# Performance work log

Measured on AMD Instinct MI355X. Metric: run time of the kernel, lower is better.

Reference implementation:

```python
import jax, jax.numpy as jnp
import numpy as np

N_NODES = 50000
N_EDGES = 600000
D_IN = 128
DIMS = [128, 128, 128]
LEAKY_SLOPE = 0.01  # torch nn.LeakyReLU default


def setup_inputs() -> dict:
    key = jax.random.key(0)
    ks = jax.random.split(key, 10)
    feat = jax.random.uniform(ks[0], (N_NODES, D_IN), dtype=jnp.float32) + 1e-3
    edge_index = jax.random.randint(ks[1], (2, N_EDGES), 0, N_NODES, dtype=jnp.int64)
    edge_weight = jax.random.uniform(ks[2], (N_EDGES,), dtype=jnp.float32) + 1e-3
    # 3 GCNConv layers: x @ W ([c_in, c_out]) then scatter-aggregate, then + bias
    scale1 = 1.0 / np.sqrt(D_IN)
    W1 = jax.random.normal(ks[3], (D_IN, DIMS[0]), dtype=jnp.float32) * scale1
    b1 = jnp.zeros((DIMS[0],), dtype=jnp.float32)
    W2 = jax.random.normal(ks[4], (DIMS[0], DIMS[1]), dtype=jnp.float32) * (1.0 / np.sqrt(DIMS[0]))
    b2 = jnp.zeros((DIMS[1],), dtype=jnp.float32)
    W3 = jax.random.normal(ks[5], (DIMS[1], DIMS[2]), dtype=jnp.float32) * (1.0 / np.sqrt(DIMS[1]))
    b3 = jnp.zeros((DIMS[2],), dtype=jnp.float32)
    return {"feat": feat, "edge_index": edge_index, "edge_weight": edge_weight,
            "W1": W1, "b1": b1, "W2": W2, "b2": b2, "W3": W3, "b3": b3}


def reference(feat, edge_index, edge_weight, W1, b1, W2, b2, W3, b3):
    N = feat.shape[0]
    src = edge_index[0]  # edge (i, j): A[i, j]; messages flow src -> dst
    dst = edge_index[1]
    # A_hat = D^{-1} A D^{-1}, D = diag(row sums of A)
    rowsum = jax.ops.segment_sum(edge_weight, src, num_segments=N)
    rinv = jnp.where(rowsum > 0, 1.0 / rowsum, 0.0)
    w_hat = edge_weight * rinv[src] * rinv[dst]
    # PyG gcn_norm (add_self_loops=False): deg over target, symmetric D^{-1/2} scaling
    deg = jax.ops.segment_sum(w_hat, dst, num_segments=N)
    dinv = jnp.where(deg > 0, jax.lax.rsqrt(deg), 0.0)
    norm = dinv[src] * w_hat * dinv[dst]  # cached, shared by all layers

    def gcn_conv(x, W, b):
        x = x @ W                              # [N, c_out]
        msg = norm[:, None] * x[src]           # gather + scale: [E, c_out]
        agg = jax.ops.segment_sum(msg, dst, num_segments=N)  # scatter-add
        return agg + b

    x = feat / jnp.sum(feat, axis=1, keepdims=True)  # row-normalize
    x = jax.nn.leaky_relu(gcn_conv(x, W1, b1), LEAKY_SLOPE)
    x = jax.nn.leaky_relu(gcn_conv(x, W2, b2), LEAKY_SLOPE)
    x = gcn_conv(x, W3, b3)  # final layer: no activation
    return x
```

## Files before the change

kernel.cpp:

```cpp
#include <hip/hip_runtime.h>

#define D 128
#define LEAKY 0.01f
#define SCAN_CHUNK 2048

typedef __attribute__((ext_vector_type(8))) short short8;
typedef __attribute__((ext_vector_type(4))) float f32x4;

__device__ __forceinline__ unsigned short f2bf(float f) {
    unsigned u = __float_as_uint(f);
    u += 0x7fffu + ((u >> 16) & 1u);
    return (unsigned short)(u >> 16);
}


__global__ void k_wprep(const float* __restrict__ W1, const float* __restrict__ W2,
                        const float* __restrict__ W3, unsigned short* __restrict__ wtg) {
    int tid = blockIdx.x * 256 + threadIdx.x;
    if (tid >= 3 * 128 * 16) return;
    int col = tid & 127;
    int s   = (tid >> 7) & 15;
    int w   = tid >> 11;
    const float* Ws = (w == 0) ? W1 : (w == 1) ? W2 : W3;
    unsigned un[4];
    #pragma unroll
    for (int p = 0; p < 4; p++) {
        float a = Ws[(s * 8 + 2 * p) * 128 + col];
        float b = Ws[(s * 8 + 2 * p + 1) * 128 + col];
        un[p] = (unsigned)f2bf(a) | ((unsigned)f2bf(b) << 16);
    }
    uint4 v = {un[0], un[1], un[2], un[3]};
    int byte = w * 32768 + col * 256 + ((s * 16) ^ ((col & 7) << 4));
    *(uint4*)((char*)wtg + byte) = v;
}


__global__ void k_pass1(const int* __restrict__ src, const int* __restrict__ dst,
                        const float* __restrict__ w, float* __restrict__ rowsum,
                        int* __restrict__ cnt, int* __restrict__ rank, int E) {
    int e = blockIdx.x * 256 + threadIdx.x;
    if (e >= E) return;
    atomicAdd(&rowsum[src[e]], w[e]);
    rank[e] = atomicAdd(&cnt[dst[e]], 1);
}


__global__ void k_chunk_sum(const int* __restrict__ cnt, int* __restrict__ partial, int n) {
    __shared__ int sdata[256];
    int b = blockIdx.x;
    int base = b * SCAN_CHUNK;
    int s = 0;
    for (int i = threadIdx.x; i < SCAN_CHUNK; i += 256) {
        int idx = base + i;
        s += (idx < n) ? cnt[idx] : 0;
    }
    sdata[threadIdx.x] = s;
    __syncthreads();
    for (int off = 128; off > 0; off >>= 1) {
        if (threadIdx.x < off) sdata[threadIdx.x] += sdata[threadIdx.x + off];
        __syncthreads();
    }
    if (threadIdx.x == 0) partial[b] = sdata[0];
}

__global__ void k_scan_partial(int* __restrict__ partial, int nchunks) {
    if (blockIdx.x == 0 && threadIdx.x == 0) {
        int run = 0;
        for (int i = 0; i < nchunks; i++) { int v = partial[i]; partial[i] = run; run += v; }
    }
}

__global__ void k_chunk_scan(const int* __restrict__ cnt, const int* __restrict__ partial,
                             int* __restrict__ start, int n, int total) {
    __shared__ int sdata[256];
    int b = blockIdx.x;
    int base = b * SCAN_CHUNK;
    int t = threadIdx.x;
    int loc[8];
    int s = 0;
    int tb = base + t * 8;
    #pragma unroll
    for (int j = 0; j < 8; j++) {
        int idx = tb + j;
        int v = (idx < n) ? cnt[idx] : 0;
        loc[j] = s;
        s += v;
    }
    sdata[t] = s;
    __syncthreads();
    for (int off = 1; off < 256; off <<= 1) {
        int v = (t >= off) ? sdata[t - off] : 0;
        __syncthreads();
        sdata[t] += v;
        __syncthreads();
    }
    int texcl = (t == 0) ? 0 : sdata[t - 1];
    int offb = partial[b];
    #pragma unroll
    for (int j = 0; j < 8; j++) {
        int idx = tb + j;
        if (idx < n) start[idx] = offb + texcl + loc[j];
    }
    if (b == gridDim.x - 1 && t == 255) start[n] = total;
}


__global__ void k_scatter2(const int* __restrict__ src, const int* __restrict__ dst,
                           const float* __restrict__ w, const float* __restrict__ rowsum,
                           const int* __restrict__ start, const int* __restrict__ rank,
                           int2* __restrict__ csr, int E) {
    int e = blockIdx.x * 256 + threadIdx.x;
    if (e >= E) return;
    int s = src[e], d = dst[e];
    float rs = rowsum[s], rd = rowsum[d];
    float wh = w[e] * (rs > 0.f ? 1.f / rs : 0.f) * (rd > 0.f ? 1.f / rd : 0.f);
    int idx = start[d] + rank[e];
    csr[idx] = make_int2(s, __float_as_int(wh));
}


__global__ void k_deg_dinv(const int2* __restrict__ csr, const int* __restrict__ start,
                           float* __restrict__ dinv, int N) {
    int n = blockIdx.x * 256 + threadIdx.x;
    if (n >= N) return;
    int s0 = start[n], s1 = start[n + 1];
    float s = 0.f;
    for (int i = s0; i < s1; i++) s += __int_as_float(csr[i].y);
    dinv[n] = s > 0.f ? rsqrtf(s) : 0.f;
}


#define GR 64

template<int DO_NORM>
__global__ __launch_bounds__(256) void k_gemm_mfma(const float* __restrict__ Xf32,
                                                   const unsigned short* __restrict__ Xb,
                                                   const unsigned short* __restrict__ Wtg,
                                                   unsigned short* __restrict__ Yb, int nrows) {
    __shared__ unsigned short Wt[128 * 128];
    __shared__ unsigned short Xs[GR * 128];
    int t = threadIdx.x;
    int rowbase = blockIdx.x * GR;

    {
        const uint4* Wg = (const uint4*)Wtg;
        uint4* Wl = (uint4*)Wt;
        #pragma unroll
        for (int i = 0; i < 8; i++) Wl[t + i * 256] = Wg[t + i * 256];
    }

    if (DO_NORM) {
        int r = t >> 2, q = t & 3;
        int row = rowbase + r;
        const float4* Xr = (const float4*)(Xf32 + (size_t)row * 128);
        float4 v[8];
        float s = 0.f;
        #pragma unroll
        for (int k = 0; k < 8; k++) {
            float4 x = make_float4(0.f, 0.f, 0.f, 0.f);
            if (row < nrows) x = Xr[q + k * 4];
            v[k] = x;
            s += x.x + x.y + x.z + x.w;
        }
        s += __shfl_down(s, 2, 4);
        s += __shfl_down(s, 1, 4);
        float tot = __shfl(s, 0, 4);
        float inv = tot > 0.f ? 1.f / tot : 0.f;
        int sw = (r & 7) << 4;
        #pragma unroll
        for (int k = 0; k < 8; k++) {
            int gidx = q + k * 4;
            ushort4 h;
            h.x = f2bf(v[k].x * inv); h.y = f2bf(v[k].y * inv);
            h.z = f2bf(v[k].z * inv); h.w = f2bf(v[k].w * inv);
            *(ushort4*)((char*)Xs + r * 256 + ((gidx * 8) ^ sw)) = h;
        }
    } else {
        for (int i = t; i < GR * 16; i += 256) {
            int r = i >> 4, c = i & 15;
            uint4 vv = {0u, 0u, 0u, 0u};
            int row = rowbase + r;
            if (row < nrows) vv = *(const uint4*)(Xb + (size_t)row * 128 + c * 8);
            int byte = r * 256 + ((c * 16) ^ ((r & 7) << 4));
            *(uint4*)((char*)Xs + byte) = vv;
        }
    }
    __syncthreads();

    int w = t >> 6, l = t & 63;
    int r0 = w * 16;
    int lr = l & 15, lg = l >> 4;

    short8 a[4];
    {
        int row = r0 + lr;
        const char* rp = (const char*)Xs + row * 256;
        int sw = (row & 7) << 4;
        #pragma unroll
        for (int s = 0; s < 4; s++)
            a[s] = *(const short8*)(rp + ((s * 64 + lg * 16) ^ sw));
    }

    f32x4 acc[8];
    #pragma unroll
    for (int ct = 0; ct < 8; ct++) {
        f32x4 c = {0.f, 0.f, 0.f, 0.f};
        int col = ct * 16 + lr;
        const char* cp = (const char*)Wt + col * 256;
        int sw = (col & 7) << 4;
        #pragma unroll
        for (int s = 0; s < 4; s++) {
            short8 b = *(const short8*)(cp + ((s * 64 + lg * 16) ^ sw));
            c = __builtin_amdgcn_mfma_f32_16x16x32_bf16(a[s], b, c, 0, 0, 0);
        }
        acc[ct] = c;
    }

    #pragma unroll
    for (int j = 0; j < 4; j++) {
        int row = rowbase + r0 + lg * 4 + j;
        if (row < nrows) {
            #pragma unroll
            for (int ct = 0; ct < 8; ct++)
                Yb[(size_t)row * 128 + ct * 16 + lr] = f2bf(acc[ct][j]);
        }
    }
}


__device__ __forceinline__ void fma8(float* acc, float n, uint4 v) {
    acc[0] += n * __uint_as_float(v.x << 16);
    acc[1] += n * __uint_as_float(v.x & 0xffff0000u);
    acc[2] += n * __uint_as_float(v.y << 16);
    acc[3] += n * __uint_as_float(v.y & 0xffff0000u);
    acc[4] += n * __uint_as_float(v.z << 16);
    acc[5] += n * __uint_as_float(v.z & 0xffff0000u);
    acc[6] += n * __uint_as_float(v.w << 16);
    acc[7] += n * __uint_as_float(v.w & 0xffff0000u);
}

template<int NORM, int FINAL>
__global__ void k_agg(const unsigned short* __restrict__ Yb, int2* __restrict__ csr,
                      const int* __restrict__ start, const float* __restrict__ dinv,
                      const float* __restrict__ bias,
                      unsigned short* __restrict__ OutB, float* __restrict__ OutF, int N) {
    int wid = (blockIdx.x * blockDim.x + threadIdx.x) >> 6;
    int lane = threadIdx.x & 63;
    int g = lane >> 4;
    int l = lane & 15;
    int node = wid * 4 + g;
    bool valid = node < N;
    int s0 = valid ? start[node] : 0;
    int s1 = valid ? start[node + 1] : 0;
    int cnt = s1 - s0;
    float ddst = 0.f;
    if (NORM) ddst = valid ? dinv[node] : 0.f;

    float acc[8] = {};
    const uint4* Y4 = (const uint4*)Yb;

    for (int base = 0; base < cnt; base += 16) {
        int rem = cnt - base; if (rem > 16) rem = 16;
        int eidx = s0 + base + l;
        int2 pr = (l < rem) ? csr[eidx] : make_int2(0, 0);
        int  sj = pr.x;
        float nj = __int_as_float(pr.y);
        if (NORM) {
            nj = nj * dinv[sj] * ddst;
            if (l < rem) csr[eidx] = make_int2(sj, __float_as_int(nj));
        }
        int j = 0;
        for (; j + 8 <= rem; j += 8) {
            int   i0 = __shfl(sj, j + 0, 16), i1 = __shfl(sj, j + 1, 16);
            int   i2 = __shfl(sj, j + 2, 16), i3 = __shfl(sj, j + 3, 16);
            int   i4 = __shfl(sj, j + 4, 16), i5 = __shfl(sj, j + 5, 16);
            int   i6 = __shfl(sj, j + 6, 16), i7 = __shfl(sj, j + 7, 16);
            float n0 = __shfl(nj, j + 0, 16), n1 = __shfl(nj, j + 1, 16);
            float n2 = __shfl(nj, j + 2, 16), n3 = __shfl(nj, j + 3, 16);
            float n4 = __shfl(nj, j + 4, 16), n5 = __shfl(nj, j + 5, 16);
            float n6 = __shfl(nj, j + 6, 16), n7 = __shfl(nj, j + 7, 16);
            uint4 v0 = Y4[(size_t)i0 * 16 + l];
            uint4 v1 = Y4[(size_t)i1 * 16 + l];
            uint4 v2 = Y4[(size_t)i2 * 16 + l];
            uint4 v3 = Y4[(size_t)i3 * 16 + l];
            uint4 v4 = Y4[(size_t)i4 * 16 + l];
            uint4 v5 = Y4[(size_t)i5 * 16 + l];
            uint4 v6 = Y4[(size_t)i6 * 16 + l];
            uint4 v7 = Y4[(size_t)i7 * 16 + l];
            fma8(acc, n0, v0); fma8(acc, n1, v1);
            fma8(acc, n2, v2); fma8(acc, n3, v3);
            fma8(acc, n4, v4); fma8(acc, n5, v5);
            fma8(acc, n6, v6); fma8(acc, n7, v7);
        }
        for (; j + 4 <= rem; j += 4) {
            int   i0 = __shfl(sj, j + 0, 16), i1 = __shfl(sj, j + 1, 16);
            int   i2 = __shfl(sj, j + 2, 16), i3 = __shfl(sj, j + 3, 16);
            float n0 = __shfl(nj, j + 0, 16), n1 = __shfl(nj, j + 1, 16);
            float n2 = __shfl(nj, j + 2, 16), n3 = __shfl(nj, j + 3, 16);
            uint4 v0 = Y4[(size_t)i0 * 16 + l];
            uint4 v1 = Y4[(size_t)i1 * 16 + l];
            uint4 v2 = Y4[(size_t)i2 * 16 + l];
            uint4 v3 = Y4[(size_t)i3 * 16 + l];
            fma8(acc, n0, v0); fma8(acc, n1, v1);
            fma8(acc, n2, v2); fma8(acc, n3, v3);
        }
        for (; j < rem; j++) {
            int   i0 = __shfl(sj, j, 16);
            float n0 = __shfl(nj, j, 16);
            uint4 v0 = Y4[(size_t)i0 * 16 + l];
            fma8(acc, n0, v0);
        }
    }

    if (!valid) return;
    float4 ba = ((const float4*)bias)[l * 2];
    float4 bb = ((const float4*)bias)[l * 2 + 1];
    float o[8];
    o[0] = acc[0] + ba.x; o[1] = acc[1] + ba.y; o[2] = acc[2] + ba.z; o[3] = acc[3] + ba.w;
    o[4] = acc[4] + bb.x; o[5] = acc[5] + bb.y; o[6] = acc[6] + bb.z; o[7] = acc[7] + bb.w;
    if (FINAL) {
        float4 w0 = {o[0], o[1], o[2], o[3]};
        float4 w1 = {o[4], o[5], o[6], o[7]};
        ((float4*)OutF)[(size_t)node * 32 + l * 2] = w0;
        ((float4*)OutF)[(size_t)node * 32 + l * 2 + 1] = w1;
    } else {
        #pragma unroll
        for (int k = 0; k < 8; k++) o[k] = o[k] > 0.f ? o[k] : LEAKY * o[k];
        uint4 ov;
        ov.x = (unsigned)f2bf(o[0]) | ((unsigned)f2bf(o[1]) << 16);
        ov.y = (unsigned)f2bf(o[2]) | ((unsigned)f2bf(o[3]) << 16);
        ov.z = (unsigned)f2bf(o[4]) | ((unsigned)f2bf(o[5]) << 16);
        ov.w = (unsigned)f2bf(o[6]) | ((unsigned)f2bf(o[7]) << 16);
        ((uint4*)OutB)[(size_t)node * 16 + l] = ov;
    }
}


extern "C" void kernel_launch(void* const* d_in, const int* in_sizes, int n_in,
                              void* d_out, int out_size, void* d_ws, size_t ws_size,
                              hipStream_t stream) {
    const float* feat = (const float*)d_in[0];
    const int*   eidx = (const int*)d_in[1];
    const float* ew   = (const float*)d_in[2];
    const float* W1   = (const float*)d_in[3];
    const float* b1   = (const float*)d_in[4];
    const float* W2   = (const float*)d_in[5];
    const float* b2   = (const float*)d_in[6];
    const float* W3   = (const float*)d_in[7];
    const float* b3   = (const float*)d_in[8];

    const int N = in_sizes[0] / D;
    const int E = in_sizes[2];
    const int* src = eidx;
    const int* dst = eidx + E;

    size_t off = 0;
    char* base = (char*)d_ws;
    auto alloc4 = [&](size_t elems) -> void* {
        void* p = base + off * 4;
        off += (elems + 3) & ~(size_t)3;
        return p;
    };
    float* rowsum = (float*)alloc4(N);
    int*   cnt    = (int*)  alloc4(N);
    char*  zero_end = base + off * 4;
    int*   start  = (int*)  alloc4(N + 1);
    float* dinv   = (float*)alloc4(N);
    int*   partial= (int*)  alloc4(64);
    int*   rank   = (int*)  alloc4(E);
    int2*  csr    = (int2*) alloc4((size_t)E * 2);
    unsigned short* wtg = (unsigned short*)alloc4(24576);
    unsigned short* xb  = (unsigned short*)alloc4((size_t)N * 64);
    unsigned short* yb  = (unsigned short*)alloc4((size_t)N * 64);
    float* outp = (float*)d_out;

    hipMemsetAsync(rowsum, 0, (size_t)(zero_end - (char*)rowsum), stream);

    int eblocks = (E + 255) / 256;
    int nchunks = (N + SCAN_CHUNK - 1) / SCAN_CHUNK;
    int nblocks = (N + 255) / 256;
    int ablocks = (((N + 3) / 4) * 64 + 255) / 256;
    int gblocks = (N + GR - 1) / GR;

    k_wprep<<<24, 256, 0, stream>>>(W1, W2, W3, wtg);
    k_pass1<<<eblocks, 256, 0, stream>>>(src, dst, ew, rowsum, cnt, rank, E);

    k_chunk_sum<<<nchunks, 256, 0, stream>>>(cnt, partial, N);
    k_scan_partial<<<1, 64, 0, stream>>>(partial, nchunks);
    k_chunk_scan<<<nchunks, 256, 0, stream>>>(cnt, partial, start, N, E);

    k_scatter2<<<eblocks, 256, 0, stream>>>(src, dst, ew, rowsum, start, rank, csr, E);
    k_deg_dinv<<<nblocks, 256, 0, stream>>>(csr, start, dinv, N);

    k_gemm_mfma<1><<<gblocks, 256, 0, stream>>>(feat, nullptr, wtg, xb, N);
    k_agg<1, 0><<<ablocks, 256, 0, stream>>>(xb, csr, start, dinv, b1, yb, nullptr, N);
    k_gemm_mfma<0><<<gblocks, 256, 0, stream>>>(nullptr, yb, wtg + 16384, yb, N);
    k_agg<0, 0><<<ablocks, 256, 0, stream>>>(yb, csr, start, nullptr, b2, xb, nullptr, N);
    k_gemm_mfma<0><<<gblocks, 256, 0, stream>>>(nullptr, xb, wtg + 32768, xb, N);
    k_agg<0, 1><<<ablocks, 256, 0, stream>>>(xb, csr, start, nullptr, b3, nullptr, outp, N);
}
```

Baseline: 302.0 us.

## Fuse aggregation with next layer's GEMM via shared-memory tile

Aggregation for layers 1 and 2 is merged with the following layer's MFMA GEMM. Each block aggregates 64 nodes, applies bias and LeakyReLU, writes the bf16 rows into a swizzled LDS tile, then multiplies by the next weight matrix. This removes one intermediate global write/read and two kernel launches. In exchange, blocks now hold 48KB of LDS and each 16-lane group walks four nodes in sequence, which reduces parallelism for the latency-bound gather.

```diff
diff --git a/kernel.cpp b/kernel.cpp
--- a/kernel.cpp
+++ b/kernel.cpp
@@ -130,104 +130,6 @@
 }
 
 
-#define GR 64
-
-template<int DO_NORM>
-__global__ __launch_bounds__(256) void k_gemm_mfma(const float* __restrict__ Xf32,
-                                                   const unsigned short* __restrict__ Xb,
-                                                   const unsigned short* __restrict__ Wtg,
-                                                   unsigned short* __restrict__ Yb, int nrows) {
-    __shared__ unsigned short Wt[128 * 128];
-    __shared__ unsigned short Xs[GR * 128];
-    int t = threadIdx.x;
-    int rowbase = blockIdx.x * GR;
-
-    {
-        const uint4* Wg = (const uint4*)Wtg;
-        uint4* Wl = (uint4*)Wt;
-        #pragma unroll
-        for (int i = 0; i < 8; i++) Wl[t + i * 256] = Wg[t + i * 256];
-    }
-
-    if (DO_NORM) {
-        int r = t >> 2, q = t & 3;
-        int row = rowbase + r;
-        const float4* Xr = (const float4*)(Xf32 + (size_t)row * 128);
-        float4 v[8];
-        float s = 0.f;
-        #pragma unroll
-        for (int k = 0; k < 8; k++) {
-            float4 x = make_float4(0.f, 0.f, 0.f, 0.f);
-            if (row < nrows) x = Xr[q + k * 4];
-            v[k] = x;
-            s += x.x + x.y + x.z + x.w;
-        }
-        s += __shfl_down(s, 2, 4);
-        s += __shfl_down(s, 1, 4);
-        float tot = __shfl(s, 0, 4);
-        float inv = tot > 0.f ? 1.f / tot : 0.f;
-        int sw = (r & 7) << 4;
-        #pragma unroll
-        for (int k = 0; k < 8; k++) {
-            int gidx = q + k * 4;
-            ushort4 h;
-            h.x = f2bf(v[k].x * inv); h.y = f2bf(v[k].y * inv);
-            h.z = f2bf(v[k].z * inv); h.w = f2bf(v[k].w * inv);
-            *(ushort4*)((char*)Xs + r * 256 + ((gidx * 8) ^ sw)) = h;
-        }
-    } else {
-        for (int i = t; i < GR * 16; i += 256) {
-            int r = i >> 4, c = i & 15;
-            uint4 vv = {0u, 0u, 0u, 0u};
-            int row = rowbase + r;
-            if (row < nrows) vv = *(const uint4*)(Xb + (size_t)row * 128 + c * 8);
-            int byte = r * 256 + ((c * 16) ^ ((r & 7) << 4));
-            *(uint4*)((char*)Xs + byte) = vv;
-        }
-    }
-    __syncthreads();
-
-    int w = t >> 6, l = t & 63;
-    int r0 = w * 16;
-    int lr = l & 15, lg = l >> 4;
-
-    short8 a[4];
-    {
-        int row = r0 + lr;
-        const char* rp = (const char*)Xs + row * 256;
-        int sw = (row & 7) << 4;
-        #pragma unroll
-        for (int s = 0; s < 4; s++)
-            a[s] = *(const short8*)(rp + ((s * 64 + lg * 16) ^ sw));
-    }
-
-    f32x4 acc[8];
-    #pragma unroll
-    for (int ct = 0; ct < 8; ct++) {
-        f32x4 c = {0.f, 0.f, 0.f, 0.f};
-        int col = ct * 16 + lr;
-        const char* cp = (const char*)Wt + col * 256;
-        int sw = (col & 7) << 4;
-        #pragma unroll
-        for (int s = 0; s < 4; s++) {
-            short8 b = *(const short8*)(cp + ((s * 64 + lg * 16) ^ sw));
-            c = __builtin_amdgcn_mfma_f32_16x16x32_bf16(a[s], b, c, 0, 0, 0);
-        }
-        acc[ct] = c;
-    }
-
-    #pragma unroll
-    for (int j = 0; j < 4; j++) {
-        int row = rowbase + r0 + lg * 4 + j;
-        if (row < nrows) {
-            #pragma unroll
-            for (int ct = 0; ct < 8; ct++)
-                Yb[(size_t)row * 128 + ct * 16 + lr] = f2bf(acc[ct][j]);
-        }
-    }
-}
-
-
 __device__ __forceinline__ void fma8(float* acc, float n, uint4 v) {
     acc[0] += n * __uint_as_float(v.x << 16);
     acc[1] += n * __uint_as_float(v.x & 0xffff0000u);
@@ -239,26 +141,11 @@
     acc[7] += n * __uint_as_float(v.w & 0xffff0000u);
 }
 
-template<int NORM, int FINAL>
-__global__ void k_agg(const unsigned short* __restrict__ Yb, int2* __restrict__ csr,
-                      const int* __restrict__ start, const float* __restrict__ dinv,
-                      const float* __restrict__ bias,
-                      unsigned short* __restrict__ OutB, float* __restrict__ OutF, int N) {
-    int wid = (blockIdx.x * blockDim.x + threadIdx.x) >> 6;
-    int lane = threadIdx.x & 63;
-    int g = lane >> 4;
-    int l = lane & 15;
-    int node = wid * 4 + g;
-    bool valid = node < N;
-    int s0 = valid ? start[node] : 0;
-    int s1 = valid ? start[node + 1] : 0;
-    int cnt = s1 - s0;
-    float ddst = 0.f;
-    if (NORM) ddst = valid ? dinv[node] : 0.f;
-
-    float acc[8] = {};
-    const uint4* Y4 = (const uint4*)Yb;
-
+template<int NORM>
+__device__ __forceinline__ void agg_accum(const uint4* __restrict__ Y4, int2* __restrict__ csr,
+                                          int s0, int cnt, int l,
+                                          const float* __restrict__ dinv, float ddst,
+                                          float* acc) {
     for (int base = 0; base < cnt; base += 16) {
         int rem = cnt - base; if (rem > 16) rem = 16;
         int eidx = s0 + base + l;
@@ -311,19 +198,54 @@
             fma8(acc, n0, v0);
         }
     }
-
-    if (!valid) return;
+}
+
+
+template<int NORM>
+__global__ __launch_bounds__(256) void k_agg_gemm(const unsigned short* __restrict__ Yb_prev,
+                                                  int2* __restrict__ csr,
+                                                  const int* __restrict__ start,
+                                                  const float* __restrict__ dinv,
+                                                  const float* __restrict__ bias,
+                                                  const unsigned short* __restrict__ Wtg,
+                                                  unsigned short* __restrict__ Yb_out, int N) {
+    __shared__ unsigned short Wt[128 * 128];
+    __shared__ unsigned short Xs[64 * 128];
+    int t = threadIdx.x;
+    int rowbase = blockIdx.x * 64;
+
+    {
+        const uint4* Wg = (const uint4*)Wtg;
+        uint4* Wl = (uint4*)Wt;
+        #pragma unroll
+        for (int i = 0; i < 8; i++) Wl[t + i * 256] = Wg[t + i * 256];
+    }
+
+    int lane = t & 63;
+    int wv = t >> 6;
+    int g = lane >> 4;
+    int l = lane & 15;
+    int G = wv * 4 + g;
+    const uint4* Y4 = (const uint4*)Yb_prev;
     float4 ba = ((const float4*)bias)[l * 2];
     float4 bb = ((const float4*)bias)[l * 2 + 1];
-    float o[8];
-    o[0] = acc[0] + ba.x; o[1] = acc[1] + ba.y; o[2] = acc[2] + ba.z; o[3] = acc[3] + ba.w;
-    o[4] = acc[4] + bb.x; o[5] = acc[5] + bb.y; o[6] = acc[6] + bb.z; o[7] = acc[7] + bb.w;
-    if (FINAL) {
-        float4 w0 = {o[0], o[1], o[2], o[3]};
-        float4 w1 = {o[4], o[5], o[6], o[7]};
-        ((float4*)OutF)[(size_t)node * 32 + l * 2] = w0;
-        ((float4*)OutF)[(size_t)node * 32 + l * 2 + 1] = w1;
-    } else {
+
+    for (int i = 0; i < 4; i++) {
+        int r = G * 4 + i;
+        int node = rowbase + r;
+        bool valid = node < N;
+        int s0 = valid ? start[node] : 0;
+        int s1 = valid ? start[node + 1] : 0;
+        int cnt = s1 - s0;
+        float ddst = 0.f;
+        if (NORM) ddst = valid ? dinv[node] : 0.f;
+
+        float acc[8] = {};
+        agg_accum<NORM>(Y4, csr, s0, cnt, l, dinv, ddst, acc);
+
+        float o[8];
+        o[0] = acc[0] + ba.x; o[1] = acc[1] + ba.y; o[2] = acc[2] + ba.z; o[3] = acc[3] + ba.w;
+        o[4] = acc[4] + bb.x; o[5] = acc[5] + bb.y; o[6] = acc[6] + bb.z; o[7] = acc[7] + bb.w;
         #pragma unroll
         for (int k = 0; k < 8; k++) o[k] = o[k] > 0.f ? o[k] : LEAKY * o[k];
         uint4 ov;
@@ -331,8 +253,161 @@
         ov.y = (unsigned)f2bf(o[2]) | ((unsigned)f2bf(o[3]) << 16);
         ov.z = (unsigned)f2bf(o[4]) | ((unsigned)f2bf(o[5]) << 16);
         ov.w = (unsigned)f2bf(o[6]) | ((unsigned)f2bf(o[7]) << 16);
-        ((uint4*)OutB)[(size_t)node * 16 + l] = ov;
-    }
+        int byte = r * 256 + ((l * 16) ^ ((r & 7) << 4));
+        *(uint4*)((char*)Xs + byte) = ov;
+    }
+    __syncthreads();
+
+    int r0 = wv * 16;
+    int lr = lane & 15, lg = lane >> 4;
+
+    short8 a[4];
+    {
+        int row = r0 + lr;
+        const char* rp = (const char*)Xs + row * 256;
+        int sw = (row & 7) << 4;
+        #pragma unroll
+        for (int s = 0; s < 4; s++)
+            a[s] = *(const short8*)(rp + ((s * 64 + lg * 16) ^ sw));
+    }
+
+    f32x4 accv[8];
+    #pragma unroll
+    for (int ct = 0; ct < 8; ct++) {
+        f32x4 c = {0.f, 0.f, 0.f, 0.f};
+        int col = ct * 16 + lr;
+        const char* cp = (const char*)Wt + col * 256;
+        int sw = (col & 7) << 4;
+        #pragma unroll
+        for (int s = 0; s < 4; s++) {
+            short8 b = *(const short8*)(cp + ((s * 64 + lg * 16) ^ sw));
+            c = __builtin_amdgcn_mfma_f32_16x16x32_bf16(a[s], b, c, 0, 0, 0);
+        }
+        accv[ct] = c;
+    }
+
+    #pragma unroll
+    for (int j = 0; j < 4; j++) {
+        int row = rowbase + r0 + lg * 4 + j;
+        if (row < N) {
+            #pragma unroll
+            for (int ct = 0; ct < 8; ct++)
+                Yb_out[(size_t)row * 128 + ct * 16 + lr] = f2bf(accv[ct][j]);
+        }
+    }
+}
+
+
+#define GR 64
+
+__global__ __launch_bounds__(256) void k_gemm1(const float* __restrict__ Xf32,
+                                               const unsigned short* __restrict__ Wtg,
+                                               unsigned short* __restrict__ Yb, int nrows) {
+    __shared__ unsigned short Wt[128 * 128];
+    __shared__ unsigned short Xs[GR * 128];
+    int t = threadIdx.x;
+    int rowbase = blockIdx.x * GR;
+
+    {
+        const uint4* Wg = (const uint4*)Wtg;
+        uint4* Wl = (uint4*)Wt;
+        #pragma unroll
+        for (int i = 0; i < 8; i++) Wl[t + i * 256] = Wg[t + i * 256];
+    }
+
+    {
+        int r = t >> 2, q = t & 3;
+        int row = rowbase + r;
+        const float4* Xr = (const float4*)(Xf32 + (size_t)row * 128);
+        float4 v[8];
+        float s = 0.f;
+        #pragma unroll
+        for (int k = 0; k < 8; k++) {
+            float4 x = make_float4(0.f, 0.f, 0.f, 0.f);
+            if (row < nrows) x = Xr[q + k * 4];
+            v[k] = x;
+            s += x.x + x.y + x.z + x.w;
+        }
+        s += __shfl_down(s, 2, 4);
+        s += __shfl_down(s, 1, 4);
+        float tot = __shfl(s, 0, 4);
+        float inv = tot > 0.f ? 1.f / tot : 0.f;
+        int sw = (r & 7) << 4;
+        #pragma unroll
+        for (int k = 0; k < 8; k++) {
+            int gidx = q + k * 4;
+            ushort4 h;
+            h.x = f2bf(v[k].x * inv); h.y = f2bf(v[k].y * inv);
+            h.z = f2bf(v[k].z * inv); h.w = f2bf(v[k].w * inv);
+            *(ushort4*)((char*)Xs + r * 256 + ((gidx * 8) ^ sw)) = h;
+        }
+    }
+    __syncthreads();
+
+    int w = t >> 6, l = t & 63;
+    int r0 = w * 16;
+    int lr = l & 15, lg = l >> 4;
+
+    short8 a[4];
+    {
+        int row = r0 + lr;
+        const char* rp = (const char*)Xs + row * 256;
+        int sw = (row & 7) << 4;
+        #pragma unroll
+        for (int s = 0; s < 4; s++)
+            a[s] = *(const short8*)(rp + ((s * 64 + lg * 16) ^ sw));
+    }
+
+    f32x4 acc[8];
+    #pragma unroll
+    for (int ct = 0; ct < 8; ct++) {
+        f32x4 c = {0.f, 0.f, 0.f, 0.f};
+        int col = ct * 16 + lr;
+        const char* cp = (const char*)Wt + col * 256;
+        int sw = (col & 7) << 4;
+        #pragma unroll
+        for (int s = 0; s < 4; s++) {
+            short8 b = *(const short8*)(cp + ((s * 64 + lg * 16) ^ sw));
+            c = __builtin_amdgcn_mfma_f32_16x16x32_bf16(a[s], b, c, 0, 0, 0);
+        }
+        acc[ct] = c;
+    }
+
+    #pragma unroll
+    for (int j = 0; j < 4; j++) {
+        int row = rowbase + r0 + lg * 4 + j;
+        if (row < nrows) {
+            #pragma unroll
+            for (int ct = 0; ct < 8; ct++)
+                Yb[(size_t)row * 128 + ct * 16 + lr] = f2bf(acc[ct][j]);
+        }
+    }
+}
+
+
+__global__ void k_agg_final(const unsigned short* __restrict__ Yb, int2* __restrict__ csr,
+                            const int* __restrict__ start, const float* __restrict__ bias,
+                            float* __restrict__ OutF, int N) {
+    int wid = (blockIdx.x * blockDim.x + threadIdx.x) >> 6;
+    int lane = threadIdx.x & 63;
+    int g = lane >> 4;
+    int l = lane & 15;
+    int node = wid * 4 + g;
+    bool valid = node < N;
+    int s0 = valid ? start[node] : 0;
+    int s1 = valid ? start[node + 1] : 0;
+    int cnt = s1 - s0;
+
+    float acc[8] = {};
+    agg_accum<0>((const uint4*)Yb, csr, s0, cnt, l, nullptr, 0.f, acc);
+
+    if (!valid) return;
+    float4 ba = ((const float4*)bias)[l * 2];
+    float4 bb = ((const float4*)bias)[l * 2 + 1];
+    float4 w0 = {acc[0] + ba.x, acc[1] + ba.y, acc[2] + ba.z, acc[3] + ba.w};
+    float4 w1 = {acc[4] + bb.x, acc[5] + bb.y, acc[6] + bb.z, acc[7] + bb.w};
+    ((float4*)OutF)[(size_t)node * 32 + l * 2] = w0;
+    ((float4*)OutF)[(size_t)node * 32 + l * 2 + 1] = w1;
 }
 
 
@@ -380,7 +455,7 @@
     int nchunks = (N + SCAN_CHUNK - 1) / SCAN_CHUNK;
     int nblocks = (N + 255) / 256;
     int ablocks = (((N + 3) / 4) * 64 + 255) / 256;
-    int gblocks = (N + GR - 1) / GR;
+    int gblocks = (N + 63) / 64;
 
     k_wprep<<<24, 256, 0, stream>>>(W1, W2, W3, wtg);
     k_pass1<<<eblocks, 256, 0, stream>>>(src, dst, ew, rowsum, cnt, rank, E);
@@ -392,10 +467,8 @@
     k_scatter2<<<eblocks, 256, 0, stream>>>(src, dst, ew, rowsum, start, rank, csr, E);
     k_deg_dinv<<<nblocks, 256, 0, stream>>>(csr, start, dinv, N);
 
-    k_gemm_mfma<1><<<gblocks, 256, 0, stream>>>(feat, nullptr, wtg, xb, N);
-    k_agg<1, 0><<<ablocks, 256, 0, stream>>>(xb, csr, start, dinv, b1, yb, nullptr, N);
-    k_gemm_mfma<0><<<gblocks, 256, 0, stream>>>(nullptr, yb, wtg + 16384, yb, N);
-    k_agg<0, 0><<<ablocks, 256, 0, stream>>>(yb, csr, start, nullptr, b2, xb, nullptr, N);
-    k_gemm_mfma<0><<<gblocks, 256, 0, stream>>>(nullptr, xb, wtg + 32768, xb, N);
-    k_agg<0, 1><<<ablocks, 256, 0, stream>>>(xb, csr, start, nullptr, b3, nullptr, outp, N);
-}
+    k_gemm1<<<gblocks, 256, 0, stream>>>(feat, wtg, xb, N);
+    k_agg_gemm<1><<<gblocks, 256, 0, stream>>>(xb, csr, start, dinv, b1, wtg + 16384, yb, N);
+    k_agg_gemm<0><<<gblocks, 256, 0, stream>>>(yb, csr, start, nullptr, b2, wtg + 32768, xb, N);
+    k_agg_final<<<ablocks, 256, 0, stream>>>(xb, csr, start, b3, outp, N);
+}
```

Result: slower. 314.3 us (+4.1%).

## Replace stored edge ranks with atomic decrement slots and fully unroll aggregation gathers

Applied to the files above, without the earlier changes.

Pass 1 no longer writes a per-edge rank array. The scatter kernel instead claims a CSR slot by atomically decrementing the per-destination count, which removes a write and a read of an E-sized array at the cost of a second round of atomics. The aggregation inner loop is also replaced by a helper that always issues 16 gathers per chunk, with masked lanes fetching row 0 at weight zero, to raise memory-level parallelism. This makes CSR order within a row nondeterministic and wastes gathers on rows with low degree.

```diff
diff --git a/kernel.cpp b/kernel.cpp
--- a/kernel.cpp
+++ b/kernel.cpp
@@ -37,11 +37,11 @@
 
 __global__ void k_pass1(const int* __restrict__ src, const int* __restrict__ dst,
                         const float* __restrict__ w, float* __restrict__ rowsum,
-                        int* __restrict__ cnt, int* __restrict__ rank, int E) {
+                        int* __restrict__ cnt, int E) {
     int e = blockIdx.x * 256 + threadIdx.x;
     if (e >= E) return;
     atomicAdd(&rowsum[src[e]], w[e]);
-    rank[e] = atomicAdd(&cnt[dst[e]], 1);
+    atomicAdd(&cnt[dst[e]], 1);
 }
 
 
@@ -107,14 +107,15 @@
 
 __global__ void k_scatter2(const int* __restrict__ src, const int* __restrict__ dst,
                            const float* __restrict__ w, const float* __restrict__ rowsum,
-                           const int* __restrict__ start, const int* __restrict__ rank,
+                           const int* __restrict__ start, int* __restrict__ cnt,
                            int2* __restrict__ csr, int E) {
     int e = blockIdx.x * 256 + threadIdx.x;
     if (e >= E) return;
     int s = src[e], d = dst[e];
     float rs = rowsum[s], rd = rowsum[d];
     float wh = w[e] * (rs > 0.f ? 1.f / rs : 0.f) * (rd > 0.f ? 1.f / rd : 0.f);
-    int idx = start[d] + rank[e];
+    int p = atomicSub(&cnt[d], 1) - 1;
+    int idx = start[d] + p;
     csr[idx] = make_int2(s, __float_as_int(wh));
 }
 
@@ -127,104 +128,6 @@
     float s = 0.f;
     for (int i = s0; i < s1; i++) s += __int_as_float(csr[i].y);
     dinv[n] = s > 0.f ? rsqrtf(s) : 0.f;
-}
-
-
-#define GR 64
-
-template<int DO_NORM>
-__global__ __launch_bounds__(256) void k_gemm_mfma(const float* __restrict__ Xf32,
-                                                   const unsigned short* __restrict__ Xb,
-                                                   const unsigned short* __restrict__ Wtg,
-                                                   unsigned short* __restrict__ Yb, int nrows) {
-    __shared__ unsigned short Wt[128 * 128];
-    __shared__ unsigned short Xs[GR * 128];
-    int t = threadIdx.x;
-    int rowbase = blockIdx.x * GR;
-
-    {
-        const uint4* Wg = (const uint4*)Wtg;
-        uint4* Wl = (uint4*)Wt;
-        #pragma unroll
-        for (int i = 0; i < 8; i++) Wl[t + i * 256] = Wg[t + i * 256];
-    }
-
-    if (DO_NORM) {
-        int r = t >> 2, q = t & 3;
-        int row = rowbase + r;
-        const float4* Xr = (const float4*)(Xf32 + (size_t)row * 128);
-        float4 v[8];
-        float s = 0.f;
-        #pragma unroll
-        for (int k = 0; k < 8; k++) {
-            float4 x = make_float4(0.f, 0.f, 0.f, 0.f);
-            if (row < nrows) x = Xr[q + k * 4];
-            v[k] = x;
-            s += x.x + x.y + x.z + x.w;
-        }
-        s += __shfl_down(s, 2, 4);
-        s += __shfl_down(s, 1, 4);
-        float tot = __shfl(s, 0, 4);
-        float inv = tot > 0.f ? 1.f / tot : 0.f;
-        int sw = (r & 7) << 4;
-        #pragma unroll
-        for (int k = 0; k < 8; k++) {
-            int gidx = q + k * 4;
-            ushort4 h;
-            h.x = f2bf(v[k].x * inv); h.y = f2bf(v[k].y * inv);
-            h.z = f2bf(v[k].z * inv); h.w = f2bf(v[k].w * inv);
-            *(ushort4*)((char*)Xs + r * 256 + ((gidx * 8) ^ sw)) = h;
-        }
-    } else {
-        for (int i = t; i < GR * 16; i += 256) {
-            int r = i >> 4, c = i & 15;
-            uint4 vv = {0u, 0u, 0u, 0u};
-            int row = rowbase + r;
-            if (row < nrows) vv = *(const uint4*)(Xb + (size_t)row * 128 + c * 8);
-            int byte = r * 256 + ((c * 16) ^ ((r & 7) << 4));
-            *(uint4*)((char*)Xs + byte) = vv;
-        }
-    }
-    __syncthreads();
-
-    int w = t >> 6, l = t & 63;
-    int r0 = w * 16;
-    int lr = l & 15, lg = l >> 4;
-
-    short8 a[4];
-    {
-        int row = r0 + lr;
-        const char* rp = (const char*)Xs + row * 256;
-        int sw = (row & 7) << 4;
-        #pragma unroll
-        for (int s = 0; s < 4; s++)
-            a[s] = *(const short8*)(rp + ((s * 64 + lg * 16) ^ sw));
-    }
-
-    f32x4 acc[8];
-    #pragma unroll
-    for (int ct = 0; ct < 8; ct++) {
-        f32x4 c = {0.f, 0.f, 0.f, 0.f};
-        int col = ct * 16 + lr;
-        const char* cp = (const char*)Wt + col * 256;
-        int sw = (col & 7) << 4;
-        #pragma unroll
-        for (int s = 0; s < 4; s++) {
-            short8 b = *(const short8*)(cp + ((s * 64 + lg * 16) ^ sw));
-            c = __builtin_amdgcn_mfma_f32_16x16x32_bf16(a[s], b, c, 0, 0, 0);
-        }
-        acc[ct] = c;
-    }
-
-    #pragma unroll
-    for (int j = 0; j < 4; j++) {
-        int row = rowbase + r0 + lg * 4 + j;
-        if (row < nrows) {
-            #pragma unroll
-            for (int ct = 0; ct < 8; ct++)
-                Yb[(size_t)row * 128 + ct * 16 + lr] = f2bf(acc[ct][j]);
-        }
-    }
 }
 
 
@@ -238,6 +141,36 @@
     acc[6] += n * __uint_as_float(v.w << 16);
     acc[7] += n * __uint_as_float(v.w & 0xffff0000u);
 }
+
+template<int NORM>
+__device__ __forceinline__ void agg_accum(const uint4* __restrict__ Y4, int2* __restrict__ csr,
+                                          int s0, int cnt, int l,
+                                          const float* __restrict__ dinv, float ddst,
+                                          float* acc) {
+    for (int base = 0; base < cnt; base += 16) {
+        int rem = cnt - base; if (rem > 16) rem = 16;
+        int eidx = s0 + base + l;
+        int2 pr = (l < rem) ? csr[eidx] : make_int2(0, 0);
+        int  sj = pr.x;
+        float nj = __int_as_float(pr.y);
+        if (NORM) {
+            nj = nj * dinv[sj] * ddst;
+            if (l < rem) csr[eidx] = make_int2(sj, __float_as_int(nj));
+        }
+        int idx[16]; float nn[16];
+        #pragma unroll
+        for (int j = 0; j < 16; j++) {
+            idx[j] = __shfl(sj, j, 16);
+            nn[j]  = __shfl(nj, j, 16);
+        }
+        uint4 v[16];
+        #pragma unroll
+        for (int j = 0; j < 16; j++) v[j] = Y4[(size_t)idx[j] * 16 + l];
+        #pragma unroll
+        for (int j = 0; j < 16; j++) fma8(acc, nn[j], v[j]);
+    }
+}
+
 
 template<int NORM, int FINAL>
 __global__ void k_agg(const unsigned short* __restrict__ Yb, int2* __restrict__ csr,
@@ -257,60 +190,7 @@
     if (NORM) ddst = valid ? dinv[node] : 0.f;
 
     float acc[8] = {};
-    const uint4* Y4 = (const uint4*)Yb;
-
-    for (int base = 0; base < cnt; base += 16) {
-        int rem = cnt - base; if (rem > 16) rem = 16;
-        int eidx = s0 + base + l;
-        int2 pr = (l < rem) ? csr[eidx] : make_int2(0, 0);
-        int  sj = pr.x;
-        float nj = __int_as_float(pr.y);
-        if (NORM) {
-            nj = nj * dinv[sj] * ddst;
-            if (l < rem) csr[eidx] = make_int2(sj, __float_as_int(nj));
-        }
-        int j = 0;
-        for (; j + 8 <= rem; j += 8) {
-            int   i0 = __shfl(sj, j + 0, 16), i1 = __shfl(sj, j + 1, 16);
-            int   i2 = __shfl(sj, j + 2, 16), i3 = __shfl(sj, j + 3, 16);
-            int   i4 = __shfl(sj, j + 4, 16), i5 = __shfl(sj, j + 5, 16);
-            int   i6 = __shfl(sj, j + 6, 16), i7 = __shfl(sj, j + 7, 16);
-            float n0 = __shfl(nj, j + 0, 16), n1 = __shfl(nj, j + 1, 16);
-            float n2 = __shfl(nj, j + 2, 16), n3 = __shfl(nj, j + 3, 16);
-            float n4 = __shfl(nj, j + 4, 16), n5 = __shfl(nj, j + 5, 16);
-            float n6 = __shfl(nj, j + 6, 16), n7 = __shfl(nj, j + 7, 16);
-            uint4 v0 = Y4[(size_t)i0 * 16 + l];
-            uint4 v1 = Y4[(size_t)i1 * 16 + l];
-            uint4 v2 = Y4[(size_t)i2 * 16 + l];
-            uint4 v3 = Y4[(size_t)i3 * 16 + l];
-            uint4 v4 = Y4[(size_t)i4 * 16 + l];
-            uint4 v5 = Y4[(size_t)i5 * 16 + l];
-            uint4 v6 = Y4[(size_t)i6 * 16 + l];
-            uint4 v7 = Y4[(size_t)i7 * 16 + l];
-            fma8(acc, n0, v0); fma8(acc, n1, v1);
-            fma8(acc, n2, v2); fma8(acc, n3, v3);
-            fma8(acc, n4, v4); fma8(acc, n5, v5);
-            fma8(acc, n6, v6); fma8(acc, n7, v7);
-        }
-        for (; j + 4 <= rem; j += 4) {
-            int   i0 = __shfl(sj, j + 0, 16), i1 = __shfl(sj, j + 1, 16);
-            int   i2 = __shfl(sj, j + 2, 16), i3 = __shfl(sj, j + 3, 16);
-            float n0 = __shfl(nj, j + 0, 16), n1 = __shfl(nj, j + 1, 16);
-            float n2 = __shfl(nj, j + 2, 16), n3 = __shfl(nj, j + 3, 16);
-            uint4 v0 = Y4[(size_t)i0 * 16 + l];
-            uint4 v1 = Y4[(size_t)i1 * 16 + l];
-            uint4 v2 = Y4[(size_t)i2 * 16 + l];
-            uint4 v3 = Y4[(size_t)i3 * 16 + l];
-            fma8(acc, n0, v0); fma8(acc, n1, v1);
-            fma8(acc, n2, v2); fma8(acc, n3, v3);
-        }
-        for (; j < rem; j++) {
-            int   i0 = __shfl(sj, j, 16);
-            float n0 = __shfl(nj, j, 16);
-            uint4 v0 = Y4[(size_t)i0 * 16 + l];
-            fma8(acc, n0, v0);
-        }
-    }
+    agg_accum<NORM>((const uint4*)Yb, csr, s0, cnt, l, dinv, ddst, acc);
 
     if (!valid) return;
     float4 ba = ((const float4*)bias)[l * 2];
@@ -332,6 +212,104 @@
         ov.z = (unsigned)f2bf(o[4]) | ((unsigned)f2bf(o[5]) << 16);
         ov.w = (unsigned)f2bf(o[6]) | ((unsigned)f2bf(o[7]) << 16);
         ((uint4*)OutB)[(size_t)node * 16 + l] = ov;
+    }
+}
+
+
+#define GR 64
+
+template<int DO_NORM>
+__global__ __launch_bounds__(256) void k_gemm_mfma(const float* __restrict__ Xf32,
+                                                   const unsigned short* __restrict__ Xb,
+                                                   const unsigned short* __restrict__ Wtg,
+                                                   unsigned short* __restrict__ Yb, int nrows) {
+    __shared__ unsigned short Wt[128 * 128];
+    __shared__ unsigned short Xs[GR * 128];
+    int t = threadIdx.x;
+    int rowbase = blockIdx.x * GR;
+
+    {
+        const uint4* Wg = (const uint4*)Wtg;
+        uint4* Wl = (uint4*)Wt;
+        #pragma unroll
+        for (int i = 0; i < 8; i++) Wl[t + i * 256] = Wg[t + i * 256];
+    }
+
+    if (DO_NORM) {
+        int r = t >> 2, q = t & 3;
+        int row = rowbase + r;
+        const float4* Xr = (const float4*)(Xf32 + (size_t)row * 128);
+        float4 v[8];
+        float s = 0.f;
+        #pragma unroll
+        for (int k = 0; k < 8; k++) {
+            float4 x = make_float4(0.f, 0.f, 0.f, 0.f);
+            if (row < nrows) x = Xr[q + k * 4];
+            v[k] = x;
+            s += x.x + x.y + x.z + x.w;
+        }
+        s += __shfl_down(s, 2, 4);
+        s += __shfl_down(s, 1, 4);
+        float tot = __shfl(s, 0, 4);
+        float inv = tot > 0.f ? 1.f / tot : 0.f;
+        int sw = (r & 7) << 4;
+        #pragma unroll
+        for (int k = 0; k < 8; k++) {
+            int gidx = q + k * 4;
+            ushort4 h;
+            h.x = f2bf(v[k].x * inv); h.y = f2bf(v[k].y * inv);
+            h.z = f2bf(v[k].z * inv); h.w = f2bf(v[k].w * inv);
+            *(ushort4*)((char*)Xs + r * 256 + ((gidx * 8) ^ sw)) = h;
+        }
+    } else {
+        for (int i = t; i < GR * 16; i += 256) {
+            int r = i >> 4, c = i & 15;
+            uint4 vv = {0u, 0u, 0u, 0u};
+            int row = rowbase + r;
+            if (row < nrows) vv = *(const uint4*)(Xb + (size_t)row * 128 + c * 8);
+            int byte = r * 256 + ((c * 16) ^ ((r & 7) << 4));
+            *(uint4*)((char*)Xs + byte) = vv;
+        }
+    }
+    __syncthreads();
+
+    int w = t >> 6, l = t & 63;
+    int r0 = w * 16;
+    int lr = l & 15, lg = l >> 4;
+
+    short8 a[4];
+    {
+        int row = r0 + lr;
+        const char* rp = (const char*)Xs + row * 256;
+        int sw = (row & 7) << 4;
+        #pragma unroll
+        for (int s = 0; s < 4; s++)
+            a[s] = *(const short8*)(rp + ((s * 64 + lg * 16) ^ sw));
+    }
+
+    f32x4 acc[8];
+    #pragma unroll
+    for (int ct = 0; ct < 8; ct++) {
+        f32x4 c = {0.f, 0.f, 0.f, 0.f};
+        int col = ct * 16 + lr;
+        const char* cp = (const char*)Wt + col * 256;
+        int sw = (col & 7) << 4;
+        #pragma unroll
+        for (int s = 0; s < 4; s++) {
+            short8 b = *(const short8*)(cp + ((s * 64 + lg * 16) ^ sw));
+            c = __builtin_amdgcn_mfma_f32_16x16x32_bf16(a[s], b, c, 0, 0, 0);
+        }
+        acc[ct] = c;
+    }
+
+    #pragma unroll
+    for (int j = 0; j < 4; j++) {
+        int row = rowbase + r0 + lg * 4 + j;
+        if (row < nrows) {
+            #pragma unroll
+            for (int ct = 0; ct < 8; ct++)
+                Yb[(size_t)row * 128 + ct * 16 + lr] = f2bf(acc[ct][j]);
+        }
     }
 }
 
@@ -367,7 +345,6 @@
     int*   start  = (int*)  alloc4(N + 1);
     float* dinv   = (float*)alloc4(N);
     int*   partial= (int*)  alloc4(64);
-    int*   rank   = (int*)  alloc4(E);
     int2*  csr    = (int2*) alloc4((size_t)E * 2);
     unsigned short* wtg = (unsigned short*)alloc4(24576);
     unsigned short* xb  = (unsigned short*)alloc4((size_t)N * 64);
@@ -383,13 +360,13 @@
     int gblocks = (N + GR - 1) / GR;
 
     k_wprep<<<24, 256, 0, stream>>>(W1, W2, W3, wtg);
-    k_pass1<<<eblocks, 256, 0, stream>>>(src, dst, ew, rowsum, cnt, rank, E);
+    k_pass1<<<eblocks, 256, 0, stream>>>(src, dst, ew, rowsum, cnt, E);
 
     k_chunk_sum<<<nchunks, 256, 0, stream>>>(cnt, partial, N);
     k_scan_partial<<<1, 64, 0, stream>>>(partial, nchunks);
     k_chunk_scan<<<nchunks, 256, 0, stream>>>(cnt, partial, start, N, E);
 
-    k_scatter2<<<eblocks, 256, 0, stream>>>(src, dst, ew, rowsum, start, rank, csr, E);
+    k_scatter2<<<eblocks, 256, 0, stream>>>(src, dst, ew, rowsum, start, cnt, csr, E);
     k_deg_dinv<<<nblocks, 256, 0, stream>>>(csr, start, dinv, N);
 
     k_gemm_mfma<1><<<gblocks, 256, 0, stream>>>(feat, nullptr, wtg, xb, N);
```

New measurement: 316.2 us. +4.7%, slower.
